# Performance work log

Measured on AMD Instinct MI355X. Metric: run time of the kernel, lower is better.

Reference implementation:

```python
import jax, jax.numpy as jnp
import numpy as np

B, N, D_IN, D_OUT = 2, 4096, 768, 768


def setup_inputs() -> dict:
    key = jax.random.key(0)
    kx, kq, kk, kv = jax.random.split(key, 4)
    x = jax.random.normal(kx, (B, N, D_IN), dtype=jnp.float32)
    # Linear(d_in, d_out, bias=False) weights, stored as [d_in, d_out]
    scale = 1.0 / np.sqrt(D_IN)
    Wq = jax.random.normal(kq, (D_IN, D_OUT), dtype=jnp.float32) * scale
    Wk = jax.random.normal(kk, (D_IN, D_OUT), dtype=jnp.float32) * scale
    Wv = jax.random.normal(kv, (D_IN, D_OUT), dtype=jnp.float32) * scale
    return {"x": x, "Wq": Wq, "Wk": Wk, "Wv": Wv}


def reference(x, Wq, Wk, Wv):
    # q,k,v: [B, N, D_OUT]
    q = jnp.einsum('bnd,de->bne', x, Wq)
    k = jnp.einsum('bnd,de->bne', x, Wk)
    v = jnp.einsum('bnd,de->bne', x, Wv)
    # Full [B, N, N] score matrix (naive attention, as in source).
    # NOTE: source's masked_fill is non-in-place and discarded, so NO causal
    # mask is actually applied -- reproduced faithfully here.
    scores = jnp.einsum('bqe,bke->bqk', q, k) / jnp.sqrt(jnp.float32(k.shape[-1]))
    weights = jax.nn.softmax(scores, axis=-1)
    # dropout rate 0.0 / eval mode -> identity
    out = jnp.einsum('bqk,bke->bqe', weights, v)  # [B, N, D_OUT]
    return out
```

## Files before the change

### kernel.cpp

```cpp
#include <hip/hip_runtime.h>

typedef __bf16 bf16x8 __attribute__((ext_vector_type(8)));
typedef float f32x4 __attribute__((ext_vector_type(4)));
typedef unsigned short us8 __attribute__((ext_vector_type(8)));

#define GAS __attribute__((address_space(1)))
#define LAS __attribute__((address_space(3)))

__device__ __forceinline__ unsigned short f32_to_bf16(float f) {
    unsigned int u = __float_as_uint(f);
    u += 0x7FFFu + ((u >> 16) & 1u);
    return (unsigned short)(u >> 16);
}

__device__ __forceinline__ float bf16_to_f32(unsigned short h) {
    return __uint_as_float((unsigned int)h << 16);
}

__device__ __forceinline__ void load16(const unsigned short* g, unsigned short* l) {
    __builtin_amdgcn_global_load_lds((GAS unsigned int*)g, (LAS unsigned int*)l, 16, 0, 0);
}

__global__ __launch_bounds__(1024) void prep(
    const float* __restrict__ x, unsigned short* __restrict__ Xbf,
    const float* __restrict__ W0, const float* __restrict__ W1, const float* __restrict__ W2,
    unsigned short* __restrict__ T0, unsigned short* __restrict__ T1, unsigned short* __restrict__ T2)
{
    __shared__ float tile[32][33];
    const int id = blockIdx.x;
    const int t = threadIdx.x;
    if (id < 1536) {
        int i = id * 1024 + t;
        float4 v = ((const float4*)x)[i];
        ushort4 o;
        o.x = f32_to_bf16(v.x); o.y = f32_to_bf16(v.y);
        o.z = f32_to_bf16(v.z); o.w = f32_to_bf16(v.w);
        ((ushort4*)Xbf)[i] = o;
    } else {
        const int tid = id - 1536;
        const int z = tid / 576, rem = tid % 576;
        const int by = rem / 24, bx = rem % 24;
        const float* W = (z == 0) ? W0 : (z == 1) ? W1 : W2;
        unsigned short* T = (z == 0) ? T0 : (z == 1) ? T1 : T2;
        const int r0 = by * 32, c0 = bx * 32;
        const int tx = t & 31, ty = t >> 5;
        tile[ty][tx] = W[(size_t)(r0 + ty) * 768 + c0 + tx];
        __syncthreads();
        T[(size_t)(c0 + ty) * 768 + r0 + tx] = f32_to_bf16(tile[tx][ty]);
    }
}

__global__ __launch_bounds__(512) void qk2(
    const unsigned short* __restrict__ Xbf,
    const unsigned short* __restrict__ Wqk,
    unsigned short* __restrict__ Qb,
    unsigned short* __restrict__ Kb)
{
    const int f = blockIdx.x;
    const int xcd = f & 7;
    const int local = f >> 3;
    const int mb = xcd * 4 + (local >> 3);
    const int nb = local & 7;
    const unsigned short* A = Xbf;
    const unsigned short* B = Wqk;
    unsigned short* C = (nb < 4) ? Qb : Kb;
    const int m0 = mb * 256;
    const int n0 = nb * 192;
    const int c0 = (nb & 3) * 192;
    const int lda = 768, ldb = 768, ldc = 768;
    constexpr int NT = 12;

    __shared__ unsigned short As[2][256 * 64];
    __shared__ unsigned short Bs[2][192 * 64];

    const int t = threadIdx.x;
    const int lane = t & 63;
    const int w = t >> 6;
    const int wm = (w >> 2) * 128;
    const int wn = (w & 3) * 48;
    const int r15 = lane & 15;
    const int qa = lane >> 4;

    const unsigned short* srcA[4];
    int dstA[4];
#pragma unroll
    for (int i = 0; i < 4; ++i) {
        const int c = i * 512 + t;
        const int row = c >> 3;
        const int cc = (c & 7) ^ (row & 7);
        srcA[i] = A + (size_t)(m0 + row) * lda + cc * 8;
        dstA[i] = c * 8;
    }
    const unsigned short* srcB[3];
    int dstB[3];
#pragma unroll
    for (int i = 0; i < 3; ++i) {
        const int c = i * 512 + t;
        const int row = c >> 3;
        const int cc = (c & 7) ^ (row & 7);
        srcB[i] = B + (size_t)(n0 + row) * ldb + cc * 8;
        dstB[i] = c * 8;
    }

    auto stage = [&](int buf, int kbase) {
#pragma unroll
        for (int i = 0; i < 4; ++i) load16(srcA[i] + kbase, &As[buf][dstA[i]]);
#pragma unroll
        for (int i = 0; i < 3; ++i) load16(srcB[i] + kbase, &Bs[buf][dstB[i]]);
    };

    int offA[8][2], offB[3][2];
#pragma unroll
    for (int mi = 0; mi < 8; ++mi) {
        const int row = wm + mi * 16 + r15;
#pragma unroll
        for (int ks = 0; ks < 2; ++ks)
            offA[mi][ks] = row * 64 + (((ks << 2) + qa) ^ (row & 7)) * 8;
    }
#pragma unroll
    for (int ni = 0; ni < 3; ++ni) {
        const int row = wn + ni * 16 + r15;
#pragma unroll
        for (int ks = 0; ks < 2; ++ks)
            offB[ni][ks] = row * 64 + (((ks << 2) + qa) ^ (row & 7)) * 8;
    }

    f32x4 acc[8][3];
#pragma unroll
    for (int i = 0; i < 8; ++i)
#pragma unroll
        for (int j = 0; j < 3; ++j) acc[i][j] = (f32x4){0.f, 0.f, 0.f, 0.f};

    stage(0, 0);
    stage(1, 64);

    for (int tt = 0; tt < NT; ++tt) {
        const int b = tt & 1;
        if (tt == NT - 1) {
            asm volatile("s_waitcnt vmcnt(0)" ::: "memory");
        } else {
            asm volatile("s_waitcnt vmcnt(7)" ::: "memory");
        }
        __builtin_amdgcn_s_barrier();

#pragma unroll
        for (int ks = 0; ks < 2; ++ks) {
            bf16x8 aA[8], bB[3];
#pragma unroll
            for (int i = 0; i < 8; ++i)
                aA[i] = *(const bf16x8*)&As[b][offA[i][ks]];
#pragma unroll
            for (int ni = 0; ni < 3; ++ni)
                bB[ni] = *(const bf16x8*)&Bs[b][offB[ni][ks]];
#pragma unroll
            for (int i = 0; i < 8; ++i)
#pragma unroll
                for (int ni = 0; ni < 3; ++ni)
                    acc[i][ni] = __builtin_amdgcn_mfma_f32_16x16x32_bf16(
                        aA[i], bB[ni], acc[i][ni], 0, 0, 0);
        }

        asm volatile("" ::: "memory");
        __builtin_amdgcn_s_barrier();

        if (tt + 2 < NT) stage(b, (tt + 2) << 6);
    }

    const int cr = (lane >> 4) * 4;
#pragma unroll
    for (int mi = 0; mi < 8; ++mi)
#pragma unroll
        for (int ni = 0; ni < 3; ++ni) {
            const int gm = m0 + wm + mi * 16 + cr;
            const int gn = c0 + wn + ni * 16 + r15;
#pragma unroll
            for (int r = 0; r < 4; ++r)
                C[(size_t)(gm + r) * ldc + gn] = f32_to_bf16(acc[mi][ni][r]);
        }
}

__global__ __launch_bounds__(512) void vt2(
    const unsigned short* __restrict__ WvT,
    const unsigned short* __restrict__ Xbf,
    unsigned short* __restrict__ Vt)
{
    const int f = blockIdx.x;
    const int xcd = f & 7;
    const int local = f >> 3;
    const int nb = xcd * 8 + (local >> 2);
    const int mb = local & 3;
    const unsigned short* A = WvT;
    const unsigned short* B = Xbf;
    unsigned short* C = Vt;
    const int m0 = mb * 192;
    const int n0 = nb * 128;
    const int lda = 768, ldb = 768, ldc = 8192;
    constexpr int NT = 12;

    __shared__ unsigned short As[2][192 * 64];
    __shared__ unsigned short Bs[2][128 * 64];

    const int t = threadIdx.x;
    const int lane = t & 63;
    const int w = t >> 6;
    const int wm = (w >> 2) * 96;
    const int wn = (w & 3) * 32;
    const int r15 = lane & 15;
    const int qa = lane >> 4;

    const unsigned short* srcA[3];
    int dstA[3];
#pragma unroll
    for (int i = 0; i < 3; ++i) {
        const int c = i * 512 + t;
        const int row = c >> 3;
        const int cc = (c & 7) ^ (row & 7);
        srcA[i] = A + (size_t)(m0 + row) * lda + cc * 8;
        dstA[i] = c * 8;
    }
    const unsigned short* srcB[2];
    int dstB[2];
#pragma unroll
    for (int i = 0; i < 2; ++i) {
        const int c = i * 512 + t;
        const int row = c >> 3;
        const int cc = (c & 7) ^ (row & 7);
        srcB[i] = B + (size_t)(n0 + row) * ldb + cc * 8;
        dstB[i] = c * 8;
    }

    auto stage = [&](int buf, int kbase) {
#pragma unroll
        for (int i = 0; i < 3; ++i) load16(srcA[i] + kbase, &As[buf][dstA[i]]);
#pragma unroll
        for (int i = 0; i < 2; ++i) load16(srcB[i] + kbase, &Bs[buf][dstB[i]]);
    };

    int offA[6][2], offB[2][2];
#pragma unroll
    for (int mi = 0; mi < 6; ++mi) {
        const int row = wm + mi * 16 + r15;
#pragma unroll
        for (int ks = 0; ks < 2; ++ks)
            offA[mi][ks] = row * 64 + (((ks << 2) + qa) ^ (row & 7)) * 8;
    }
#pragma unroll
    for (int ni = 0; ni < 2; ++ni) {
        const int row = wn + ni * 16 + r15;
#pragma unroll
        for (int ks = 0; ks < 2; ++ks)
            offB[ni][ks] = row * 64 + (((ks << 2) + qa) ^ (row & 7)) * 8;
    }

    f32x4 acc[6][2];
#pragma unroll
    for (int i = 0; i < 6; ++i)
#pragma unroll
        for (int j = 0; j < 2; ++j) acc[i][j] = (f32x4){0.f, 0.f, 0.f, 0.f};

    stage(0, 0);
    stage(1, 64);

    for (int tt = 0; tt < NT; ++tt) {
        const int b = tt & 1;
        if (tt == NT - 1) {
            asm volatile("s_waitcnt vmcnt(0)" ::: "memory");
        } else {
            asm volatile("s_waitcnt vmcnt(5)" ::: "memory");
        }
        __builtin_amdgcn_s_barrier();

#pragma unroll
        for (int ks = 0; ks < 2; ++ks) {
            bf16x8 aA[6], bB[2];
#pragma unroll
            for (int i = 0; i < 6; ++i)
                aA[i] = *(const bf16x8*)&As[b][offA[i][ks]];
#pragma unroll
            for (int ni = 0; ni < 2; ++ni)
                bB[ni] = *(const bf16x8*)&Bs[b][offB[ni][ks]];
#pragma unroll
            for (int i = 0; i < 6; ++i)
#pragma unroll
                for (int ni = 0; ni < 2; ++ni)
                    acc[i][ni] = __builtin_amdgcn_mfma_f32_16x16x32_bf16(
                        aA[i], bB[ni], acc[i][ni], 0, 0, 0);
        }

        asm volatile("" ::: "memory");
        __builtin_amdgcn_s_barrier();

        if (tt + 2 < NT) stage(b, (tt + 2) << 6);
    }

    const int cr = (lane >> 4) * 4;
#pragma unroll
    for (int mi = 0; mi < 6; ++mi)
#pragma unroll
        for (int ni = 0; ni < 2; ++ni) {
            const int gm = m0 + wm + mi * 16 + cr;
            const int gn = n0 + wn + ni * 16 + r15;
#pragma unroll
            for (int r = 0; r < 4; ++r)
                C[(size_t)(gm + r) * ldc + gn] = f32_to_bf16(acc[mi][ni][r]);
        }
}

__global__ __launch_bounds__(512) void gemm_s_exp2(
    const unsigned short* __restrict__ Q, const unsigned short* __restrict__ Kb,
    unsigned short* __restrict__ Sexp, float alpha)
{
    const int f = blockIdx.x;
    const int xcd = f & 7;
    const int local = f >> 3;
    const int x = (xcd & 1) * 8 + (local & 7);
    const int y = ((xcd >> 1) & 1) * 8 + (local >> 3);
    const int bb = xcd >> 2;
    const unsigned short* A = Q + (size_t)bb * 3145728;
    const unsigned short* B = Kb + (size_t)bb * 3145728;
    unsigned short* C = Sexp + (size_t)bb * 16777216;
    const int m0 = y * 256, n0 = x * 256;
    const int lda = 768, ldb = 768, ldc = 4096;
    constexpr int NT = 12;

    __shared__ unsigned short As[2][256 * 64];
    __shared__ unsigned short Bs[2][256 * 64];

    const int t = threadIdx.x;
    const int lane = t & 63;
    const int w = t >> 6;
    const int wm = (w >> 2) * 128;
    const int wn = (w & 3) * 64;
    const int r15 = lane & 15;
    const int qa = lane >> 4;

    const unsigned short* srcA[4];
    const unsigned short* srcB[4];
    int dst[4];
#pragma unroll
    for (int i = 0; i < 4; ++i) {
        const int c = i * 512 + t;
        const int row = c >> 3;
        const int cc = (c & 7) ^ (row & 7);
        srcA[i] = A + (size_t)(m0 + row) * lda + cc * 8;
        srcB[i] = B + (size_t)(n0 + row) * ldb + cc * 8;
        dst[i] = c * 8;
    }

    auto stage = [&](int buf, int kbase) {
#pragma unroll
        for (int i = 0; i < 4; ++i)
            load16(srcA[i] + kbase, &As[buf][dst[i]]);
#pragma unroll
        for (int i = 0; i < 4; ++i)
            load16(srcB[i] + kbase, &Bs[buf][dst[i]]);
    };

    int offA[8][2], offB[4][2];
#pragma unroll
    for (int mi = 0; mi < 8; ++mi) {
        const int row = wm + mi * 16 + r15;
#pragma unroll
        for (int ks = 0; ks < 2; ++ks)
            offA[mi][ks] = row * 64 + (((ks << 2) + qa) ^ (row & 7)) * 8;
    }
#pragma unroll
    for (int ni = 0; ni < 4; ++ni) {
        const int row = wn + ni * 16 + r15;
#pragma unroll
        for (int ks = 0; ks < 2; ++ks)
            offB[ni][ks] = row * 64 + (((ks << 2) + qa) ^ (row & 7)) * 8;
    }

    f32x4 acc[8][4];
#pragma unroll
    for (int i = 0; i < 8; ++i)
#pragma unroll
        for (int j = 0; j < 4; ++j) acc[i][j] = (f32x4){0.f, 0.f, 0.f, 0.f};

    stage(0, 0);
    stage(1, 64);

    for (int tt = 0; tt < NT; ++tt) {
        const int b = tt & 1;
        if (tt == NT - 1) {
            asm volatile("s_waitcnt vmcnt(0)" ::: "memory");
        } else {
            asm volatile("s_waitcnt vmcnt(8)" ::: "memory");
        }
        __builtin_amdgcn_s_barrier();

#pragma unroll
        for (int ks = 0; ks < 2; ++ks) {
            bf16x8 aA[8], bB[4];
#pragma unroll
            for (int i = 0; i < 8; ++i)
                aA[i] = *(const bf16x8*)&As[b][offA[i][ks]];
#pragma unroll
            for (int ni = 0; ni < 4; ++ni)
                bB[ni] = *(const bf16x8*)&Bs[b][offB[ni][ks]];
#pragma unroll
            for (int i = 0; i < 8; ++i)
#pragma unroll
                for (int ni = 0; ni < 4; ++ni)
                    acc[i][ni] = __builtin_amdgcn_mfma_f32_16x16x32_bf16(
                        aA[i], bB[ni], acc[i][ni], 0, 0, 0);
        }

        asm volatile("" ::: "memory");
        __builtin_amdgcn_s_barrier();

        if (tt + 2 < NT) stage(b, (tt + 2) << 6);
    }

    const int cr = (lane >> 4) * 4;
#pragma unroll
    for (int mi = 0; mi < 8; ++mi)
#pragma unroll
        for (int ni = 0; ni < 4; ++ni) {
            const int gm = m0 + wm + mi * 16 + cr;
            const int gn = n0 + wn + ni * 16 + r15;
#pragma unroll
            for (int r = 0; r < 4; ++r)
                C[(size_t)(gm + r) * ldc + gn] =
                    f32_to_bf16(__expf(alpha * acc[mi][ni][r]));
        }
}

__global__ __launch_bounds__(256) void rowsum(
    const unsigned short* __restrict__ Sexp, float* __restrict__ lsum)
{
    const int w = threadIdx.x >> 6;
    const int lane = threadIdx.x & 63;
    const int row = blockIdx.x * 4 + w;
    const unsigned short* rp = Sexp + (size_t)row * 4096;
    float s = 0.f;
#pragma unroll
    for (int i = 0; i < 8; ++i) {
        us8 v = ((const us8*)rp)[lane + i * 64];
#pragma unroll
        for (int j = 0; j < 8; ++j) s += bf16_to_f32(v[j]);
    }
#pragma unroll
    for (int off = 32; off > 0; off >>= 1) s += __shfl_down(s, off, 64);
    if (lane == 0) lsum[row] = s;
}

__global__ __launch_bounds__(512) void gemm_out(
    const unsigned short* __restrict__ P, const unsigned short* __restrict__ Vt,
    const float* __restrict__ lsum, float* __restrict__ out)
{
    const int f = blockIdx.x;
    const int xcd = f & 7;
    const int local = f >> 3;
    const int nb = local & 3;
    const int rg = xcd * 8 + (local >> 2);
    const int batch = rg >> 5;
    const int mb = rg & 31;
    const unsigned short* A = P + (size_t)batch * 16777216;
    const unsigned short* B = Vt + (size_t)batch * 4096;
    const float* ls = lsum + batch * 4096;
    float* C = out + (size_t)batch * 3145728;
    const int m0 = mb * 128, n0 = nb * 192;
    const int lda = 4096, ldb = 8192;
    constexpr int NT = 64;

    __shared__ unsigned short As[3][128 * 64];
    __shared__ unsigned short Bs[3][192 * 64];

    const int t = threadIdx.x;
    const int lane = t & 63;
    const int w = t >> 6;
    const int wm = (w >> 2) * 64;
    const int wn = (w & 3) * 48;
    const int r15 = lane & 15;
    const int qa = lane >> 4;

    const unsigned short* srcA[2];
    int dstA[2];
#pragma unroll
    for (int i = 0; i < 2; ++i) {
        const int c = i * 512 + t;
        const int row = c >> 3;
        const int cc = (c & 7) ^ (row & 7);
        srcA[i] = A + (size_t)(m0 + row) * lda + cc * 8;
        dstA[i] = c * 8;
    }
    const unsigned short* srcB[3];
    int dstB[3];
#pragma unroll
    for (int i = 0; i < 3; ++i) {
        const int c = i * 512 + t;
        const int row = c >> 3;
        const int cc = (c & 7) ^ (row & 7);
        srcB[i] = B + (size_t)(n0 + row) * ldb + cc * 8;
        dstB[i] = c * 8;
    }

    auto stage = [&](int buf, int kbase) {
#pragma unroll
        for (int i = 0; i < 2; ++i)
            load16(srcA[i] + kbase, &As[buf][dstA[i]]);
#pragma unroll
        for (int i = 0; i < 3; ++i)
            load16(srcB[i] + kbase, &Bs[buf][dstB[i]]);
    };

    int offA[4][2], offB[3][2];
#pragma unroll
    for (int mi = 0; mi < 4; ++mi) {
        const int row = wm + mi * 16 + r15;
#pragma unroll
        for (int ks = 0; ks < 2; ++ks)
            offA[mi][ks] = row * 64 + (((ks << 2) + qa) ^ (row & 7)) * 8;
    }
#pragma unroll
    for (int ni = 0; ni < 3; ++ni) {
        const int row = wn + ni * 16 + r15;
#pragma unroll
        for (int ks = 0; ks < 2; ++ks)
            offB[ni][ks] = row * 64 + (((ks << 2) + qa) ^ (row & 7)) * 8;
    }

    f32x4 acc[4][3];
#pragma unroll
    for (int i = 0; i < 4; ++i)
#pragma unroll
        for (int j = 0; j < 3; ++j) acc[i][j] = (f32x4){0.f, 0.f, 0.f, 0.f};

    stage(0, 0);
    stage(1, 64);
    stage(2, 128);

    int b = 0;
    for (int tt = 0; tt < NT; ++tt) {
        if (tt < NT - 2) {
            asm volatile("s_waitcnt vmcnt(10)" ::: "memory");
        } else if (tt == NT - 2) {
            asm volatile("s_waitcnt vmcnt(5)" ::: "memory");
        } else {
            asm volatile("s_waitcnt vmcnt(0)" ::: "memory");
        }
        __builtin_amdgcn_s_barrier();

#pragma unroll
        for (int ks = 0; ks < 2; ++ks) {
            bf16x8 aA[4], bB[3];
#pragma unroll
            for (int i = 0; i < 4; ++i)
                aA[i] = *(const bf16x8*)&As[b][offA[i][ks]];
#pragma unroll
            for (int ni = 0; ni < 3; ++ni)
                bB[ni] = *(const bf16x8*)&Bs[b][offB[ni][ks]];
#pragma unroll
            for (int i = 0; i < 4; ++i)
#pragma unroll
                for (int ni = 0; ni < 3; ++ni)
                    acc[i][ni] = __builtin_amdgcn_mfma_f32_16x16x32_bf16(
                        aA[i], bB[ni], acc[i][ni], 0, 0, 0);
        }

        asm volatile("" ::: "memory");
        __builtin_amdgcn_s_barrier();

        if (tt + 3 < NT) stage(b, (tt + 3) << 6);
        b = (b == 2) ? 0 : b + 1;
    }

    const int cr = (lane >> 4) * 4;
#pragma unroll
    for (int mi = 0; mi < 4; ++mi) {
        const int gm = m0 + wm + mi * 16 + cr;
        const float i0 = 1.f / ls[gm + 0];
        const float i1 = 1.f / ls[gm + 1];
        const float i2 = 1.f / ls[gm + 2];
        const float i3 = 1.f / ls[gm + 3];
#pragma unroll
        for (int ni = 0; ni < 3; ++ni) {
            const int gn = n0 + wn + ni * 16 + r15;
            C[(size_t)(gm + 0) * 768 + gn] = acc[mi][ni][0] * i0;
            C[(size_t)(gm + 1) * 768 + gn] = acc[mi][ni][1] * i1;
            C[(size_t)(gm + 2) * 768 + gn] = acc[mi][ni][2] * i2;
            C[(size_t)(gm + 3) * 768 + gn] = acc[mi][ni][3] * i3;
        }
    }
}

extern "C" void kernel_launch(void* const* d_in, const int* in_sizes, int n_in,
                              void* d_out, int out_size, void* d_ws, size_t ws_size,
                              hipStream_t stream) {
    const float* x  = (const float*)d_in[0];
    const float* Wq = (const float*)d_in[1];
    const float* Wk = (const float*)d_in[2];
    const float* Wv = (const float*)d_in[3];
    float* out = (float*)d_out;

    char* base = (char*)d_ws;
    size_t off = 0;
    auto alloc = [&](size_t b) { char* p = base + off; off += (b + 255) & ~(size_t)255; return p; };

    unsigned short* Xbf = (unsigned short*)alloc(8192ull * 768 * 2);
    unsigned short* WqT = (unsigned short*)alloc(768ull * 768 * 2);
    unsigned short* WkT = (unsigned short*)alloc(768ull * 768 * 2);
    unsigned short* WvT = (unsigned short*)alloc(768ull * 768 * 2);
    unsigned short* Qb  = (unsigned short*)alloc(8192ull * 768 * 2);
    unsigned short* Kb  = (unsigned short*)alloc(8192ull * 768 * 2);
    unsigned short* Vt  = (unsigned short*)alloc(768ull * 8192 * 2);
    unsigned short* Sexp = (unsigned short*)alloc(2ull * 4096 * 4096 * 2);
    float* lsum = (float*)alloc(2ull * 4096 * 4);
    (void)ws_size; (void)in_sizes; (void)n_in; (void)out_size; (void)WkT; (void)WvT;

    prep<<<dim3(3264), dim3(1024), 0, stream>>>(x, Xbf, Wq, Wk, Wv, WqT, WkT, WvT);
    qk2<<<dim3(256), dim3(512), 0, stream>>>(Xbf, WqT, Qb, Kb);
    vt2<<<dim3(256), dim3(512), 0, stream>>>(WvT, Xbf, Vt);
    gemm_s_exp2<<<dim3(512), dim3(512), 0, stream>>>(
        Qb, Kb, Sexp, 0.03608439182435161f);
    rowsum<<<dim3(2048), dim3(256), 0, stream>>>(Sexp, lsum);
    gemm_out<<<dim3(256), dim3(512), 0, stream>>>(Sexp, Vt, lsum, out);
}
```

Baseline: 258.0 us.

## Merge Q/K and V projection launches and fuse softmax row-sum into output GEMM

The separate qk2 and vt2 kernels become one qkv3 launch with 512 blocks. They share one dynamically partitioned LDS buffer and branch on block index. The standalone rowsum kernel is removed, so the 64 MB exp-score matrix is no longer re-read from global memory. Instead, gemm_out sums each row from the P tiles already staged in LDS, reduces the sum with shuffles and normalises from LDS. This adds per-iteration LDS reads and VALU adds inside the output GEMM loop, and the work is repeated across the column blocks.

Result: faster. 248.4 us (-3.7%).

```diff
diff --git a/kernel.cpp b/kernel.cpp
--- a/kernel.cpp
+++ b/kernel.cpp
@@ -50,17 +50,17 @@
     }
 }
 
-__global__ __launch_bounds__(512) void qk2(
-    const unsigned short* __restrict__ Xbf,
-    const unsigned short* __restrict__ Wqk,
-    unsigned short* __restrict__ Qb,
-    unsigned short* __restrict__ Kb)
+__device__ __forceinline__ void qk_body(
+    unsigned short* smem, int f,
+    const unsigned short* __restrict__ Xbf, const unsigned short* __restrict__ Wqk,
+    unsigned short* __restrict__ Qb, unsigned short* __restrict__ Kb)
 {
-    const int f = blockIdx.x;
     const int xcd = f & 7;
     const int local = f >> 3;
     const int mb = xcd * 4 + (local >> 3);
     const int nb = local & 7;
+    unsigned short* AsP[2] = { smem, smem + 16384 };
+    unsigned short* BsP[2] = { smem + 32768, smem + 32768 + 12288 };
     const unsigned short* A = Xbf;
     const unsigned short* B = Wqk;
     unsigned short* C = (nb < 4) ? Qb : Kb;
@@ -70,9 +70,6 @@
     const int lda = 768, ldb = 768, ldc = 768;
     constexpr int NT = 12;
 
-    __shared__ unsigned short As[2][256 * 64];
-    __shared__ unsigned short Bs[2][192 * 64];
-
     const int t = threadIdx.x;
     const int lane = t & 63;
     const int w = t >> 6;
@@ -104,9 +101,9 @@
 
     auto stage = [&](int buf, int kbase) {
 #pragma unroll
-        for (int i = 0; i < 4; ++i) load16(srcA[i] + kbase, &As[buf][dstA[i]]);
-#pragma unroll
-        for (int i = 0; i < 3; ++i) load16(srcB[i] + kbase, &Bs[buf][dstB[i]]);
+        for (int i = 0; i < 4; ++i) load16(srcA[i] + kbase, &AsP[buf][dstA[i]]);
+#pragma unroll
+        for (int i = 0; i < 3; ++i) load16(srcB[i] + kbase, &BsP[buf][dstB[i]]);
     };
 
     int offA[8][2], offB[3][2];
@@ -148,10 +145,10 @@
             bf16x8 aA[8], bB[3];
 #pragma unroll
             for (int i = 0; i < 8; ++i)
-                aA[i] = *(const bf16x8*)&As[b][offA[i][ks]];
+                aA[i] = *(const bf16x8*)&AsP[b][offA[i][ks]];
 #pragma unroll
             for (int ni = 0; ni < 3; ++ni)
-                bB[ni] = *(const bf16x8*)&Bs[b][offB[ni][ks]];
+                bB[ni] = *(const bf16x8*)&BsP[b][offB[ni][ks]];
 #pragma unroll
             for (int i = 0; i < 8; ++i)
 #pragma unroll
@@ -179,16 +176,17 @@
         }
 }
 
-__global__ __launch_bounds__(512) void vt2(
-    const unsigned short* __restrict__ WvT,
-    const unsigned short* __restrict__ Xbf,
+__device__ __forceinline__ void vt_body(
+    unsigned short* smem, int f,
+    const unsigned short* __restrict__ WvT, const unsigned short* __restrict__ Xbf,
     unsigned short* __restrict__ Vt)
 {
-    const int f = blockIdx.x;
     const int xcd = f & 7;
     const int local = f >> 3;
     const int nb = xcd * 8 + (local >> 2);
     const int mb = local & 3;
+    unsigned short* AsP[2] = { smem, smem + 12288 };
+    unsigned short* BsP[2] = { smem + 24576, smem + 24576 + 8192 };
     const unsigned short* A = WvT;
     const unsigned short* B = Xbf;
     unsigned short* C = Vt;
@@ -197,9 +195,6 @@
     const int lda = 768, ldb = 768, ldc = 8192;
     constexpr int NT = 12;
 
-    __shared__ unsigned short As[2][192 * 64];
-    __shared__ unsigned short Bs[2][128 * 64];
-
     const int t = threadIdx.x;
     const int lane = t & 63;
     const int w = t >> 6;
@@ -231,9 +226,9 @@
 
     auto stage = [&](int buf, int kbase) {
 #pragma unroll
-        for (int i = 0; i < 3; ++i) load16(srcA[i] + kbase, &As[buf][dstA[i]]);
-#pragma unroll
-        for (int i = 0; i < 2; ++i) load16(srcB[i] + kbase, &Bs[buf][dstB[i]]);
+        for (int i = 0; i < 3; ++i) load16(srcA[i] + kbase, &AsP[buf][dstA[i]]);
+#pragma unroll
+        for (int i = 0; i < 2; ++i) load16(srcB[i] + kbase, &BsP[buf][dstB[i]]);
     };
 
     int offA[6][2], offB[2][2];
@@ -275,10 +270,10 @@
             bf16x8 aA[6], bB[2];
 #pragma unroll
             for (int i = 0; i < 6; ++i)
-                aA[i] = *(const bf16x8*)&As[b][offA[i][ks]];
+                aA[i] = *(const bf16x8*)&AsP[b][offA[i][ks]];
 #pragma unroll
             for (int ni = 0; ni < 2; ++ni)
-                bB[ni] = *(const bf16x8*)&Bs[b][offB[ni][ks]];
+                bB[ni] = *(const bf16x8*)&BsP[b][offB[ni][ks]];
 #pragma unroll
             for (int i = 0; i < 6; ++i)
 #pragma unroll
@@ -304,6 +299,19 @@
             for (int r = 0; r < 4; ++r)
                 C[(size_t)(gm + r) * ldc + gn] = f32_to_bf16(acc[mi][ni][r]);
         }
+}
+
+__global__ __launch_bounds__(512) void qkv3(
+    const unsigned short* __restrict__ Xbf,
+    const unsigned short* __restrict__ Wqk,
+    unsigned short* __restrict__ Qb,
+    unsigned short* __restrict__ Kb,
+    unsigned short* __restrict__ Vt)
+{
+    __shared__ unsigned short smem[57344];
+    const int f = blockIdx.x;
+    if (f < 256) qk_body(smem, f, Xbf, Wqk, Qb, Kb);
+    else         vt_body(smem, f - 256, Wqk + 1179648, Xbf, Vt);
 }
 
 __global__ __launch_bounds__(512) void gemm_s_exp2(
@@ -427,28 +435,9 @@
         }
 }
 
-__global__ __launch_bounds__(256) void rowsum(
-    const unsigned short* __restrict__ Sexp, float* __restrict__ lsum)
-{
-    const int w = threadIdx.x >> 6;
-    const int lane = threadIdx.x & 63;
-    const int row = blockIdx.x * 4 + w;
-    const unsigned short* rp = Sexp + (size_t)row * 4096;
-    float s = 0.f;
-#pragma unroll
-    for (int i = 0; i < 8; ++i) {
-        us8 v = ((const us8*)rp)[lane + i * 64];
-#pragma unroll
-        for (int j = 0; j < 8; ++j) s += bf16_to_f32(v[j]);
-    }
-#pragma unroll
-    for (int off = 32; off > 0; off >>= 1) s += __shfl_down(s, off, 64);
-    if (lane == 0) lsum[row] = s;
-}
-
 __global__ __launch_bounds__(512) void gemm_out(
     const unsigned short* __restrict__ P, const unsigned short* __restrict__ Vt,
-    const float* __restrict__ lsum, float* __restrict__ out)
+    float* __restrict__ out)
 {
     const int f = blockIdx.x;
     const int xcd = f & 7;
@@ -459,7 +448,6 @@
     const int mb = rg & 31;
     const unsigned short* A = P + (size_t)batch * 16777216;
     const unsigned short* B = Vt + (size_t)batch * 4096;
-    const float* ls = lsum + batch * 4096;
     float* C = out + (size_t)batch * 3145728;
     const int m0 = mb * 128, n0 = nb * 192;
     const int lda = 4096, ldb = 8192;
@@ -467,6 +455,7 @@
 
     __shared__ unsigned short As[3][128 * 64];
     __shared__ unsigned short Bs[3][192 * 64];
+    __shared__ float lsum_lds[128];
 
     const int t = threadIdx.x;
     const int lane = t & 63;
@@ -527,6 +516,7 @@
     for (int i = 0; i < 4; ++i)
 #pragma unroll
         for (int j = 0; j < 3; ++j) acc[i][j] = (f32x4){0.f, 0.f, 0.f, 0.f};
+    float rsum = 0.f;
 
     stage(0, 0);
     stage(1, 64);
@@ -560,6 +550,14 @@
                         aA[i], bB[ni], acc[i][ni], 0, 0, 0);
         }
 
+        {
+            const us8* rp = (const us8*)&As[b][(t >> 2) * 64 + (t & 3) * 16];
+            us8 v0 = rp[0], v1 = rp[1];
+#pragma unroll
+            for (int j = 0; j < 8; ++j)
+                rsum += bf16_to_f32(v0[j]) + bf16_to_f32(v1[j]);
+        }
+
         asm volatile("" ::: "memory");
         __builtin_amdgcn_s_barrier();
 
@@ -567,14 +565,20 @@
         b = (b == 2) ? 0 : b + 1;
     }
 
+    rsum += __shfl_xor(rsum, 1, 64);
+    rsum += __shfl_xor(rsum, 2, 64);
+    if ((t & 3) == 0) lsum_lds[t >> 2] = rsum;
+    __syncthreads();
+
     const int cr = (lane >> 4) * 4;
 #pragma unroll
     for (int mi = 0; mi < 4; ++mi) {
-        const int gm = m0 + wm + mi * 16 + cr;
-        const float i0 = 1.f / ls[gm + 0];
-        const float i1 = 1.f / ls[gm + 1];
-        const float i2 = 1.f / ls[gm + 2];
-        const float i3 = 1.f / ls[gm + 3];
+        const int lr = wm + mi * 16 + cr;
+        const int gm = m0 + lr;
+        const float i0 = 1.f / lsum_lds[lr + 0];
+        const float i1 = 1.f / lsum_lds[lr + 1];
+        const float i2 = 1.f / lsum_lds[lr + 2];
+        const float i3 = 1.f / lsum_lds[lr + 3];
 #pragma unroll
         for (int ni = 0; ni < 3; ++ni) {
             const int gn = n0 + wn + ni * 16 + r15;
@@ -607,14 +611,11 @@
     unsigned short* Kb  = (unsigned short*)alloc(8192ull * 768 * 2);
     unsigned short* Vt  = (unsigned short*)alloc(768ull * 8192 * 2);
     unsigned short* Sexp = (unsigned short*)alloc(2ull * 4096 * 4096 * 2);
-    float* lsum = (float*)alloc(2ull * 4096 * 4);
     (void)ws_size; (void)in_sizes; (void)n_in; (void)out_size; (void)WkT; (void)WvT;
 
     prep<<<dim3(3264), dim3(1024), 0, stream>>>(x, Xbf, Wq, Wk, Wv, WqT, WkT, WvT);
-    qk2<<<dim3(256), dim3(512), 0, stream>>>(Xbf, WqT, Qb, Kb);
-    vt2<<<dim3(256), dim3(512), 0, stream>>>(WvT, Xbf, Vt);
+    qkv3<<<dim3(512), dim3(512), 0, stream>>>(Xbf, WqT, Qb, Kb, Vt);
     gemm_s_exp2<<<dim3(512), dim3(512), 0, stream>>>(
         Qb, Kb, Sexp, 0.03608439182435161f);
-    rowsum<<<dim3(2048), dim3(256), 0, stream>>>(Sexp, lsum);
-    gemm_out<<<dim3(256), dim3(512), 0, stream>>>(Sexp, Vt, lsum, out);
-}
+    gemm_out<<<dim3(256), dim3(512), 0, stream>>>(Sexp, Vt, out);
+}
```
